# Optimization experiments

Hardware: AMD Instinct MI355X
Metric: run time of the kernel (lower is better)

## Reference

```python
import jax, jax.numpy as jnp
import numpy as np
from jax.ops import segment_sum, segment_max

NEG_SLOPE = 0.2  # PyG GATv2Conv default

def _gatv2(x, ei, ea, Wl, bl, Wr, br, We, att, b, n):
    # PyG GATv2Conv, heads=1, concat=True, add_self_loops=True, fill_value='mean'
    src, dst = ei[0], ei[1]
    ones = jnp.ones((src.shape[0],), x.dtype)
    deg = segment_sum(ones, dst, num_segments=n)
    ea_mean = segment_sum(ea, dst, num_segments=n) / jnp.maximum(deg, 1.0)[:, None]
    loop = jnp.arange(n, dtype=src.dtype)
    src = jnp.concatenate([src, loop]); dst = jnp.concatenate([dst, loop])
    ea = jnp.concatenate([ea, ea_mean], axis=0)
    xl = x @ Wl.T + bl          # lin_l, used for both message and source term
    xr = x @ Wr.T + br          # lin_r, target term
    h = jax.nn.leaky_relu(xl[src] + xr[dst] + ea @ We.T, NEG_SLOPE)  # [E+N, F]
    logits = h @ att            # [E+N]
    m = segment_max(logits, dst, num_segments=n)   # every node has a self-loop -> finite
    p = jnp.exp(logits - m[dst])
    denom = segment_sum(p, dst, num_segments=n)
    alpha = p / denom[dst]
    return segment_sum(alpha[:, None] * xl[src], dst, num_segments=n) + b

def _mean_pool(h, seg, num):
    s = segment_sum(h, seg, num_segments=num)
    c = segment_sum(jnp.ones(h.shape[:1], h.dtype), seg, num_segments=num)
    return s / jnp.maximum(c, 1.0)[:, None]

def setup_inputs() -> dict:
    key = jax.random.key(0)
    ks = iter(jax.random.split(key, 64))
    def nrm(shape, scale=None):
        s = scale if scale is not None else 1.0 / np.sqrt(shape[-1])
        return jax.random.normal(next(ks), shape, jnp.float32) * s
    N, E = 80000, 1280000
    NR, ER, R = 20480, 40960, 512
    inp = {
        'x': nrm((N, 16), 1.0),
        'edge_attr': nrm((E, 18), 1.0),
        'rule_x': nrm((NR, 16), 1.0),
        'rule_edge_attr': nrm((ER, 18), 1.0),
    }
    def gat(fi, fo):
        return (nrm((fo, fi)), jnp.zeros(fo), nrm((fo, fi)), jnp.zeros(fo),
                nrm((fo, 18)), nrm((fo,), 1.0 / np.sqrt(fo)), jnp.zeros(fo))
    for name, (fi, fo) in [('gat0', (16, 100)), ('gat1', (16, 100)), ('gat2', (100, 200))]:
        for suf, v in zip(['Wl', 'bl', 'Wr', 'br', 'We', 'att', 'b'], gat(fi, fo)):
            inp[name + '_' + suf] = v
    inp['lin_W'] = nrm((400, 200)); inp['lin_b'] = jnp.zeros(400)
    inp['f1_W'] = nrm((200, 400)); inp['f1_b'] = jnp.zeros(200)
    inp['f2_W'] = nrm((100, 200)); inp['f2_b'] = jnp.zeros(100)
    inp['f3_W'] = nrm((100, 100)); inp['f3_b'] = jnp.zeros(100)
    inp['bil_W'] = nrm((1, 100, 100)); inp['bil_b'] = jnp.zeros(1)
    inp['edge_index'] = jax.random.randint(next(ks), (2, E), 0, N, dtype=jnp.int32)
    inp['batch'] = jnp.zeros((N,), jnp.int32)
    inp['rule_edge_index'] = jax.random.randint(next(ks), (2, ER), 0, NR, dtype=jnp.int32)
    inp['rule_batch'] = jnp.sort(jax.random.randint(next(ks), (NR,), 0, R, dtype=jnp.int32))
    inp['n_rules'] = R
    return inp

def reference(x, edge_attr, rule_x, rule_edge_attr,
              gat0_Wl, gat0_bl, gat0_Wr, gat0_br, gat0_We, gat0_att, gat0_b,
              gat1_Wl, gat1_bl, gat1_Wr, gat1_br, gat1_We, gat1_att, gat1_b,
              gat2_Wl, gat2_bl, gat2_Wr, gat2_br, gat2_We, gat2_att, gat2_b,
              lin_W, lin_b, f1_W, f1_b, f2_W, f2_b, f3_W, f3_b, bil_W, bil_b,
              edge_index, batch, rule_edge_index, rule_batch, n_rules):
    N = x.shape[0]; NR = rule_x.shape[0]
    # --- RuleParse path ---
    h = jax.nn.relu(_gatv2(rule_x, rule_edge_index, rule_edge_attr,
                           gat1_Wl, gat1_bl, gat1_Wr, gat1_br, gat1_We, gat1_att, gat1_b, NR))
    h = jax.nn.relu(_gatv2(h, rule_edge_index, rule_edge_attr,
                           gat2_Wl, gat2_bl, gat2_Wr, gat2_br, gat2_We, gat2_att, gat2_b, NR))
    h = h @ lin_W.T + lin_b                          # [NR, 400]
    y = _mean_pool(h, rule_batch, n_rules)           # [R, 400]
    y = jax.nn.relu(y @ f1_W.T + f1_b)
    y = jax.nn.relu(y @ f2_W.T + f2_b)
    y = y @ f3_W.T + f3_b                            # [R, 100]
    # --- data path ---
    g = _gatv2(x, edge_index, edge_attr,
               gat0_Wl, gat0_bl, gat0_Wr, gat0_br, gat0_We, gat0_att, gat0_b, N)
    xp = _mean_pool(g, batch, 1)                     # single graph -> [1, 100]
    xr = jnp.tile(xp, (n_rules, 1))                  # x.repeat(len(rules), 1)
    out = jnp.einsum('nd,ode,ne->no', xr, bil_W, y) + bil_b  # Bilinear(100,100,1) -> [R,1]
    return out.T.squeeze()                           # [R]
```

## Files before the change

### kernel.cpp

```cpp
#include <hip/hip_runtime.h>

#define NS 0.2f

__global__ void k_deg(const int* __restrict__ dst, int* degi, int E){
  int stride = gridDim.x * blockDim.x;
  for(int e = blockIdx.x * blockDim.x + threadIdx.x; e < E; e += stride)
    atomicAdd(&degi[dst[e]], 1);
}

__device__ __forceinline__ int wave_iscan(int v, int lane){
  #pragma unroll
  for(int o = 1; o < 64; o <<= 1){
    int t = __shfl_up(v, o);
    if(lane >= o) v += t;
  }
  return v;
}

__global__ __launch_bounds__(1024) void k_scan_sum(
    const int* __restrict__ deg, int* __restrict__ bsum, int n)
{
  __shared__ int wsum[16];
  const int lane = threadIdx.x & 63;
  const int w = threadIdx.x >> 6;
  int idx = blockIdx.x * 1024 + threadIdx.x;
  int v = (idx < n) ? deg[idx] : 0;
  #pragma unroll
  for(int o = 32; o; o >>= 1) v += __shfl_xor(v, o);
  if(lane == 0) wsum[w] = v;
  __syncthreads();
  if(w == 0){
    int s = (lane < 16) ? wsum[lane] : 0;
    #pragma unroll
    for(int o = 8; o; o >>= 1) s += __shfl_xor(s, o);
    if(lane == 0) bsum[blockIdx.x] = s;
  }
}

__global__ __launch_bounds__(128) void k_scan_bsum(
    int* __restrict__ bsum, int* __restrict__ rowoff, int B, int n)
{
  __shared__ int wtot[2];
  const int lane = threadIdx.x & 63;
  const int w = threadIdx.x >> 6;
  int t = threadIdx.x;
  int v = (t < B) ? bsum[t] : 0;
  int inc = wave_iscan(v, lane);
  if(lane == 63) wtot[w] = inc;
  __syncthreads();
  int off = (w > 0) ? wtot[0] : 0;
  if(t < B) bsum[t] = off + inc - v;
  if(t == 0) rowoff[n] = wtot[0] + wtot[1];
}

__global__ __launch_bounds__(1024) void k_scan_apply(
    const int* __restrict__ deg, const int* __restrict__ bsum,
    int* __restrict__ rowoff, int* __restrict__ pos, int n)
{
  __shared__ int wsum[16];
  const int lane = threadIdx.x & 63;
  const int w = threadIdx.x >> 6;
  int idx = blockIdx.x * 1024 + threadIdx.x;
  int v = (idx < n) ? deg[idx] : 0;
  int inc = wave_iscan(v, lane);
  if(lane == 63) wsum[w] = inc;
  __syncthreads();
  if(w == 0){
    int s = (lane < 16) ? wsum[lane] : 0;
    s = wave_iscan(s, lane);
    if(lane < 16) wsum[lane] = s;
  }
  __syncthreads();
  int woff = (w > 0) ? wsum[w - 1] : 0;
  if(idx < n){
    int ex = bsum[blockIdx.x] + woff + inc - v;
    rowoff[idx] = ex;
    pos[idx] = ex;
  }
}

__global__ void k_fill(const int* __restrict__ dst, int* pos, int* eidx, int E){
  int stride = gridDim.x * blockDim.x;
  for(int e = blockIdx.x * blockDim.x + threadIdx.x; e < E; e += stride){
    int slot = atomicAdd(&pos[dst[e]], 1);
    eidx[slot] = e;
  }
}

__global__ __launch_bounds__(256) void k_easum(
    const float* __restrict__ ea, const int* __restrict__ rowoff,
    const int* __restrict__ eidx, float* __restrict__ eam, int n)
{
  const int lane = threadIdx.x & 63;
  const int wid  = threadIdx.x >> 6;
  const int i = blockIdx.x * 4 + wid;
  if(i >= n) return;
  const int r0 = rowoff[i], r1 = rowoff[i + 1];
  const int deg = r1 - r0;
  const int pg = lane / 18;
  const int k  = lane - pg * 18;
  float s = 0.0f;
  if(pg < 3){
    for(int p = r0 + pg; p < r1; p += 3)
      s += ea[(long)eidx[p] * 18 + k];
  }
  float b = __shfl(s, lane + 18);
  float c = __shfl(s, lane + 36);
  if(lane < 18) eam[(long)i * 18 + lane] = (s + b + c) / fmaxf((float)deg, 1.0f);
}

#define BM 64
#define BN 64
#define BK 16
__global__ __launch_bounds__(256) void k_gemm(
    const float* __restrict__ A, const float* __restrict__ W,
    const float* __restrict__ b, float* __restrict__ C,
    int n, int K, int M, int dorelu)
{
  __shared__ float As[BK][BM + 4];
  __shared__ float Bs[BK][BN + 4];
  const int bi = blockIdx.x * BM;
  const int bj = blockIdx.y * BN;
  const int tid = threadIdx.x;
  const int tr = tid / 16, tc = tid % 16;
  float acc[4][4] = {};
  for(int k0 = 0; k0 < K; k0 += BK){
    for(int l = tid; l < BM * BK; l += 256){
      int c = l % BK, r = l / BK;
      int gr = bi + r, gc = k0 + c;
      As[c][r] = (gr < n && gc < K) ? A[(long)gr * K + gc] : 0.0f;
    }
    for(int l = tid; l < BN * BK; l += 256){
      int c = l % BK, r = l / BK;
      int gr = bj + r, gc = k0 + c;
      Bs[c][r] = (gr < M && gc < K) ? W[(long)gr * K + gc] : 0.0f;
    }
    __syncthreads();
    #pragma unroll
    for(int kk = 0; kk < BK; ++kk){
      float4 av = *(const float4*)&As[kk][tr * 4];
      float4 bv = *(const float4*)&Bs[kk][tc * 4];
      acc[0][0] = fmaf(av.x, bv.x, acc[0][0]); acc[0][1] = fmaf(av.x, bv.y, acc[0][1]);
      acc[0][2] = fmaf(av.x, bv.z, acc[0][2]); acc[0][3] = fmaf(av.x, bv.w, acc[0][3]);
      acc[1][0] = fmaf(av.y, bv.x, acc[1][0]); acc[1][1] = fmaf(av.y, bv.y, acc[1][1]);
      acc[1][2] = fmaf(av.y, bv.z, acc[1][2]); acc[1][3] = fmaf(av.y, bv.w, acc[1][3]);
      acc[2][0] = fmaf(av.z, bv.x, acc[2][0]); acc[2][1] = fmaf(av.z, bv.y, acc[2][1]);
      acc[2][2] = fmaf(av.z, bv.z, acc[2][2]); acc[2][3] = fmaf(av.z, bv.w, acc[2][3]);
      acc[3][0] = fmaf(av.w, bv.x, acc[3][0]); acc[3][1] = fmaf(av.w, bv.y, acc[3][1]);
      acc[3][2] = fmaf(av.w, bv.z, acc[3][2]); acc[3][3] = fmaf(av.w, bv.w, acc[3][3]);
    }
    __syncthreads();
  }
  for(int r = 0; r < 4; r++){
    int gr = bi + tr * 4 + r;
    if(gr >= n) continue;
    for(int c = 0; c < 4; c++){
      int gc = bj + tc * 4 + c;
      if(gc >= M) continue;
      float val = acc[r][c] + b[gc];
      C[(long)gr * M + gc] = dorelu ? fmaxf(val, 0.0f) : val;
    }
  }
}

static void gemm_launch(const float* A, const float* W, const float* b, float* C,
                        int n, int K, int M, int relu, hipStream_t s){
  dim3 grid((n + BM - 1) / BM, (M + BN - 1) / BN);
  k_gemm<<<grid, 256, 0, s>>>(A, W, b, C, n, K, M, relu);
}

__device__ __forceinline__ float lkrelu(float t){ return (t > 0.0f) ? t : NS * t; }

template<int G, int F>
__global__ __launch_bounds__(256) void k_edge_logits(
    const float* __restrict__ xl, const float* __restrict__ xr,
    const float* __restrict__ ea,
    const int* __restrict__ src, const int* __restrict__ dst,
    const int* __restrict__ eidx,
    const float* __restrict__ We, const float* __restrict__ att,
    float2* __restrict__ lw, int E)
{
  constexpr int NG = 256 / G;
  constexpr int NE = 4;
  constexpr int FQ = F / 4;
  __shared__ float4 sWeT[18 * FQ];
  __shared__ float4 sAtt[FQ];
  __shared__ float4 sEa[NG][18];
  __shared__ int    sIdx[NG][3][NE];

  const int tid = threadIdx.x;
  for(int idx = tid; idx < F * 18; idx += 256){
    int f = idx / 18, k = idx % 18;
    ((float*)sWeT)[k * F + f] = We[idx];
  }
  for(int f = tid; f < F; f += 256) ((float*)sAtt)[f] = att[f];
  __syncthreads();

  const int g  = tid / G;
  const int gl = tid % G;
  const bool act = (gl * 4 < F);
  const int glc = act ? gl : 0;
  const long step = (long)gridDim.x * (NG * NE);

  for(long base = (long)blockIdx.x * (NG * NE); base < (long)E; base += step){
    const long pb = base + (long)g * NE;
    if(gl < NE){
      long p = pb + gl;
      int e = -1, s = 0, d = 0;
      if(p < (long)E){ e = eidx[p]; s = src[e]; d = dst[e]; }
      sIdx[g][0][gl] = e; sIdx[g][1][gl] = s; sIdx[g][2][gl] = d;
    }
    #pragma unroll
    for(int t = 0; t < (9 * NE + G - 1) / G; ++t){
      int u = t * G + gl;
      if(u < 9 * NE){
        int ne = u & 3, k2 = u >> 2;
        int e = sIdx[g][0][ne];
        float2 v = (e >= 0) ? *(const float2*)(ea + (long)e * 18 + k2 * 2)
                            : make_float2(0.0f, 0.0f);
        ((float*)&sEa[g][k2 * 2 + 0])[ne] = v.x;
        ((float*)&sEa[g][k2 * 2 + 1])[ne] = v.y;
      }
    }
    int4 sv = *(const int4*)&sIdx[g][1][0];
    int4 dv = *(const int4*)&sIdx[g][2][0];
    float4 a0 = *(const float4*)(xl + (long)sv.x * F + glc * 4);
    float4 b0 = *(const float4*)(xr + (long)dv.x * F + glc * 4);
    float4 a1 = *(const float4*)(xl + (long)sv.y * F + glc * 4);
    float4 b1 = *(const float4*)(xr + (long)dv.y * F + glc * 4);
    float4 a2 = *(const float4*)(xl + (long)sv.z * F + glc * 4);
    float4 b2 = *(const float4*)(xr + (long)dv.z * F + glc * 4);
    float4 a3 = *(const float4*)(xl + (long)sv.w * F + glc * 4);
    float4 b3 = *(const float4*)(xr + (long)dv.w * F + glc * 4);
    float4 t0 = make_float4(a0.x + b0.x, a0.y + b0.y, a0.z + b0.z, a0.w + b0.w);
    float4 t1 = make_float4(a1.x + b1.x, a1.y + b1.y, a1.z + b1.z, a1.w + b1.w);
    float4 t2 = make_float4(a2.x + b2.x, a2.y + b2.y, a2.z + b2.z, a2.w + b2.w);
    float4 t3 = make_float4(a3.x + b3.x, a3.y + b3.y, a3.z + b3.z, a3.w + b3.w);
    #pragma unroll
    for(int k = 0; k < 18; ++k){
      float4 w  = sWeT[k * FQ + glc];
      float4 eq = sEa[g][k];
      t0.x = fmaf(w.x, eq.x, t0.x); t0.y = fmaf(w.y, eq.x, t0.y);
      t0.z = fmaf(w.z, eq.x, t0.z); t0.w = fmaf(w.w, eq.x, t0.w);
      t1.x = fmaf(w.x, eq.y, t1.x); t1.y = fmaf(w.y, eq.y, t1.y);
      t1.z = fmaf(w.z, eq.y, t1.z); t1.w = fmaf(w.w, eq.y, t1.w);
      t2.x = fmaf(w.x, eq.z, t2.x); t2.y = fmaf(w.y, eq.z, t2.y);
      t2.z = fmaf(w.z, eq.z, t2.z); t2.w = fmaf(w.w, eq.z, t2.w);
      t3.x = fmaf(w.x, eq.w, t3.x); t3.y = fmaf(w.y, eq.w, t3.y);
      t3.z = fmaf(w.z, eq.w, t3.z); t3.w = fmaf(w.w, eq.w, t3.w);
    }
    float4 av = sAtt[glc];
    float r0 = 0, r1 = 0, r2 = 0, r3 = 0;
    if(act){
      r0 = av.x * lkrelu(t0.x) + av.y * lkrelu(t0.y) + av.z * lkrelu(t0.z) + av.w * lkrelu(t0.w);
      r1 = av.x * lkrelu(t1.x) + av.y * lkrelu(t1.y) + av.z * lkrelu(t1.z) + av.w * lkrelu(t1.w);
      r2 = av.x * lkrelu(t2.x) + av.y * lkrelu(t2.y) + av.z * lkrelu(t2.z) + av.w * lkrelu(t2.w);
      r3 = av.x * lkrelu(t3.x) + av.y * lkrelu(t3.y) + av.z * lkrelu(t3.z) + av.w * lkrelu(t3.w);
    }
    #pragma unroll
    for(int o = G / 2; o; o >>= 1){
      r0 += __shfl_xor(r0, o);
      r1 += __shfl_xor(r1, o);
      r2 += __shfl_xor(r2, o);
      r3 += __shfl_xor(r3, o);
    }
    if(gl == 0 && pb + 0 < (long)E) lw[pb + 0] = make_float2(r0, __int_as_float(sv.x));
    if(gl == 1 && pb + 1 < (long)E) lw[pb + 1] = make_float2(r1, __int_as_float(sv.y));
    if(gl == 2 && pb + 2 < (long)E) lw[pb + 2] = make_float2(r2, __int_as_float(sv.z));
    if(gl == 3 && pb + 3 < (long)E) lw[pb + 3] = make_float2(r3, __int_as_float(sv.w));
  }
}

#define CH 128
template<int JMAX>
__global__ __launch_bounds__(256) void k_gat_agg(
    const float* __restrict__ xl, const float* __restrict__ xr,
    const float* __restrict__ eam,
    const float* __restrict__ We, const float* __restrict__ att,
    const int* __restrict__ rowoff, const float2* __restrict__ lw,
    const float* __restrict__ bias, float* __restrict__ out,
    int n, int F, int dorelu)
{
  const int lane = threadIdx.x & 63;
  const int wid  = threadIdx.x >> 6;
  __shared__ float2 s_ws[4][CH];
  const int i = blockIdx.x * 4 + wid;
  if(i >= n) return;
  const int r0 = rowoff[i], r1 = rowoff[i + 1];
  const int deg = r1 - r0;

  float eamv[18];
  #pragma unroll
  for(int k = 0; k < 18; ++k) eamv[k] = eam[(long)i * 18 + k];

  float selfl = 0.0f;
  float acc[JMAX];
  #pragma unroll
  for(int j = 0; j < JMAX; ++j){
    int f = lane + j * 64;
    float xv = (f < F) ? xl[(long)i * F + f] : 0.0f;
    acc[j] = xv;
    if(f < F){
      float t = xv + xr[(long)i * F + f];
      const float* w = We + f * 18;
      #pragma unroll
      for(int k = 0; k < 18; ++k) t = fmaf(w[k], eamv[k], t);
      t = lkrelu(t);
      selfl = fmaf(att[f], t, selfl);
    }
  }
  #pragma unroll
  for(int o = 32; o; o >>= 1) selfl += __shfl_xor(selfl, o);

  float m = selfl, denom = 1.0f;

  for(int c0 = 0; c0 < deg; c0 += CH){
    int cn = min(CH, deg - c0);
    float lmax = -3.4e38f;
    for(int q = lane; q < cn; q += 64){
      float2 ws = lw[r0 + c0 + q];
      s_ws[wid][q] = ws;
      lmax = fmaxf(lmax, ws.x);
    }
    #pragma unroll
    for(int o = 32; o; o >>= 1) lmax = fmaxf(lmax, __shfl_xor(lmax, o));
    float newm = fmaxf(m, lmax);
    float scale = __expf(m - newm);
    denom *= scale;
    #pragma unroll
    for(int j = 0; j < JMAX; ++j) acc[j] *= scale;
    m = newm;
    float psum = 0.0f;
    for(int q = lane; q < cn; q += 64){
      float2 ws = s_ws[wid][q];
      float w = __expf(ws.x - m);
      s_ws[wid][q].x = w;
      psum += w;
    }
    #pragma unroll
    for(int o = 32; o; o >>= 1) psum += __shfl_xor(psum, o);
    denom += psum;
    int p = 0;
    for(; p + 8 <= cn; p += 8){
      float2 wv[8];
      const float* xs[8];
      #pragma unroll
      for(int u = 0; u < 8; ++u){
        wv[u] = s_ws[wid][p + u];
        xs[u] = xl + (long)__float_as_int(wv[u].y) * F;
      }
      float vv[8][JMAX];
      #pragma unroll
      for(int u = 0; u < 8; ++u)
        #pragma unroll
        for(int j = 0; j < JMAX; ++j){
          int f = lane + j * 64;
          vv[u][j] = (f < F) ? xs[u][f] : 0.0f;
        }
      #pragma unroll
      for(int u = 0; u < 8; ++u)
        #pragma unroll
        for(int j = 0; j < JMAX; ++j)
          acc[j] = fmaf(wv[u].x, vv[u][j], acc[j]);
    }
    for(; p < cn; ++p){
      float2 ws = s_ws[wid][p];
      const float* xs = xl + (long)__float_as_int(ws.y) * F;
      #pragma unroll
      for(int j = 0; j < JMAX; ++j){
        int f = lane + j * 64;
        if(f < F) acc[j] = fmaf(ws.x, xs[f], acc[j]);
      }
    }
  }

  float inv = 1.0f / denom;
  #pragma unroll
  for(int j = 0; j < JMAX; ++j){
    int f = lane + j * 64;
    if(f < F){
      float o = acc[j] * inv + bias[f];
      out[(long)i * F + f] = dorelu ? fmaxf(o, 0.0f) : o;
    }
  }
}

__global__ void k_rule_starts(const int* __restrict__ rb, int* starts, int NR, int R){
  int r = blockIdx.x * blockDim.x + threadIdx.x;
  if(r > R) return;
  if(r == R){ starts[R] = NR; return; }
  int lo = 0, hi = NR;
  while(lo < hi){ int mid = (lo + hi) >> 1; if(rb[mid] < r) lo = mid + 1; else hi = mid; }
  starts[r] = lo;
}

__global__ void k_pool_rules(const float* __restrict__ h, const int* __restrict__ starts,
                             float* __restrict__ y, int R, int F){
  long idx = (long)blockIdx.x * blockDim.x + threadIdx.x;
  long total = (long)R * F;
  if(idx >= total) return;
  int r = (int)(idx / F);
  int f = (int)(idx % F);
  int s0 = starts[r], s1 = starts[r + 1];
  float a = 0.0f;
  for(int i = s0; i < s1; i++) a += h[(long)i * F + f];
  y[idx] = a / fmaxf((float)(s1 - s0), 1.0f);
}

__global__ __launch_bounds__(256) void k_pool_all(
    const float* __restrict__ g, float* xp, int n, int F)
{
  const int lane = threadIdx.x & 63;
  const int wid  = threadIdx.x >> 6;
  const int nw   = 4;
  float a0 = 0.0f, a1 = 0.0f;
  const bool ok0 = lane < F, ok1 = lane + 64 < F;
  for(int r = blockIdx.x * nw + wid; r < n; r += gridDim.x * nw){
    const float* row = g + (long)r * F;
    if(ok0) a0 += row[lane];
    if(ok1) a1 += row[lane + 64];
  }
  __shared__ float s[4][128];
  s[wid][lane] = a0;
  s[wid][lane + 64] = a1;
  __syncthreads();
  if(wid == 0){
    float t0 = s[0][lane] + s[1][lane] + s[2][lane] + s[3][lane];
    float t1 = s[0][lane + 64] + s[1][lane + 64] + s[2][lane + 64] + s[3][lane + 64];
    if(ok0 && t0 != 0.0f) atomicAdd(&xp[lane], t0);
    if(ok1 && t1 != 0.0f) atomicAdd(&xp[lane + 64], t1);
  }
}

__global__ __launch_bounds__(512) void k_bil(
    const float* __restrict__ xp, const float* __restrict__ Wb,
    const float* __restrict__ y, const float* __restrict__ bilb,
    float* __restrict__ out, float inv_n, int R)
{
  __shared__ float v[100];
  int t = threadIdx.x;
  if(t < 100){
    float a = 0.0f;
    for(int d = 0; d < 100; d++) a += xp[d] * Wb[d * 100 + t];
    v[t] = a * inv_n;
  }
  __syncthreads();
  for(int r = t; r < R; r += 512){
    float a = 0.0f;
    const float* yr = y + (long)r * 100;
    for(int e = 0; e < 100; e++) a += v[e] * yr[e];
    out[r] = a + bilb[0];
  }
}

static inline int nblk(long n){
  long b = (n + 255) / 256;
  if(b > 20480) b = 20480;
  if(b < 1) b = 1;
  return (int)b;
}

struct GatParams { const float *Wl,*bl,*Wr,*br,*We,*att,*b; };

template<int G, int F>
static void logits_launch(const float* xl, const float* xr, const float* ea,
                          const int* src, const int* dst, const int* eidx,
                          const float* We, const float* att, float2* lw,
                          int E, hipStream_t stream){
  const int epb = (256 / G) * 4;
  long nb = ((long)E + epb - 1) / epb;
  int grid = (int)(nb < 2048 ? nb : 2048);
  k_edge_logits<G, F><<<grid, 256, 0, stream>>>(xl, xr, ea, src, dst, eidx, We, att, lw, E);
}

static void scan_launch(const int* degi, int* bsum, int* rowoff, int* pos,
                        int n, hipStream_t stream){
  int B = (n + 1023) / 1024;
  k_scan_sum  <<<B, 1024, 0, stream>>>(degi, bsum, n);
  k_scan_bsum <<<1, 128,  0, stream>>>(bsum, rowoff, B, n);
  k_scan_apply<<<B, 1024, 0, stream>>>(degi, bsum, rowoff, pos, n);
}

static void run_gatv2(const float* x, int fin, int fout, int n,
                      const int* src, const int* dst, const float* ea, int E,
                      GatParams P, float* out, int dorelu,
                      float* xl, float* xr, float2* lw,
                      const float* eam, const int* rowoff, const int* eidx,
                      hipStream_t stream){
  gemm_launch(x, P.Wl, P.bl, xl, n, fin, fout, 0, stream);
  gemm_launch(x, P.Wr, P.br, xr, n, fin, fout, 0, stream);
  if(fout == 100){
    logits_launch<32, 100>(xl, xr, ea, src, dst, eidx, P.We, P.att, lw, E, stream);
    k_gat_agg<2><<<(n + 3) / 4, 256, 0, stream>>>(xl, xr, eam, P.We, P.att,
                                                  rowoff, lw, P.b, out, n, fout, dorelu);
  } else {
    logits_launch<64, 200>(xl, xr, ea, src, dst, eidx, P.We, P.att, lw, E, stream);
    k_gat_agg<4><<<(n + 3) / 4, 256, 0, stream>>>(xl, xr, eam, P.We, P.att,
                                                  rowoff, lw, P.b, out, n, fout, dorelu);
  }
}

extern "C" void kernel_launch(void* const* d_in, const int* in_sizes, int n_in,
                              void* d_out, int out_size, void* d_ws, size_t ws_size,
                              hipStream_t stream){
  const float* x   = (const float*)d_in[0];
  const float* ea  = (const float*)d_in[1];
  const float* rx  = (const float*)d_in[2];
  const float* rea = (const float*)d_in[3];
  GatParams g0{ (const float*)d_in[4],  (const float*)d_in[5],  (const float*)d_in[6],
                (const float*)d_in[7],  (const float*)d_in[8],  (const float*)d_in[9],
                (const float*)d_in[10] };
  GatParams g1{ (const float*)d_in[11], (const float*)d_in[12], (const float*)d_in[13],
                (const float*)d_in[14], (const float*)d_in[15], (const float*)d_in[16],
                (const float*)d_in[17] };
  GatParams g2{ (const float*)d_in[18], (const float*)d_in[19], (const float*)d_in[20],
                (const float*)d_in[21], (const float*)d_in[22], (const float*)d_in[23],
                (const float*)d_in[24] };
  const float* lin_W = (const float*)d_in[25]; const float* lin_b = (const float*)d_in[26];
  const float* f1_W  = (const float*)d_in[27]; const float* f1_b  = (const float*)d_in[28];
  const float* f2_W  = (const float*)d_in[29]; const float* f2_b  = (const float*)d_in[30];
  const float* f3_W  = (const float*)d_in[31]; const float* f3_b  = (const float*)d_in[32];
  const float* bilW  = (const float*)d_in[33]; const float* bilb  = (const float*)d_in[34];
  const int* ei  = (const int*)d_in[35];
  const int* rei = (const int*)d_in[37];
  const int* rb  = (const int*)d_in[38];

  const int N  = in_sizes[0] / 16;
  const int E  = in_sizes[1] / 18;
  const int NR = in_sizes[2] / 16;
  const int ER = in_sizes[3] / 18;
  const int R  = out_size;

  float* Wf = (float*)d_ws;
  size_t off = 0;
  auto alloc  = [&](size_t nf){ nf = (nf + 1) & ~(size_t)1; float* p = Wf + off; off += nf; return p; };
  auto alloci = [&](size_t ni){ ni = (ni + 1) & ~(size_t)1; int* p = (int*)(Wf + off); off += ni; return p; };

  float* y0 = alloc((size_t)R * 400);
  float* y1 = alloc((size_t)R * 200);
  float* y2 = alloc((size_t)R * 100);
  float* y3 = alloc((size_t)R * 100);
  float* xp = alloc(128);
  int* starts = alloci(R + 1);
  const size_t arena = off;

  {
    off = arena;
    float* h1 = alloc((size_t)NR * 100);
    float* h2 = alloc((size_t)NR * 200);
    float* xl = alloc((size_t)NR * 200);
    float* xr = alloc((size_t)NR * 200);
    float2* lw = (float2*)alloc((size_t)ER * 2);
    float* eam   = alloc((size_t)NR * 18);
    int* rowoff = alloci(NR + 1);
    int* degi   = alloci(NR);
    int* pos    = alloci(NR);
    int* bsum   = alloci(128);
    int* eidx   = alloci(ER);
    const int* rsrc = rei; const int* rdst = rei + ER;

    hipMemsetAsync(degi, 0, (size_t)NR * 4, stream);
    k_deg<<<nblk(ER), 256, 0, stream>>>(rdst, degi, ER);
    scan_launch(degi, bsum, rowoff, pos, NR, stream);
    k_fill<<<nblk(ER), 256, 0, stream>>>(rdst, pos, eidx, ER);
    k_easum<<<(NR + 3) / 4, 256, 0, stream>>>(rea, rowoff, eidx, eam, NR);

    run_gatv2(rx, 16, 100, NR, rsrc, rdst, rea, ER, g1, h1, 1,
              xl, xr, lw, eam, rowoff, eidx, stream);
    run_gatv2(h1, 100, 200, NR, rsrc, rdst, rea, ER, g2, h2, 1,
              xl, xr, lw, eam, rowoff, eidx, stream);

    float* hlin = xl;
    gemm_launch(h2, lin_W, lin_b, hlin, NR, 200, 400, 0, stream);

    k_rule_starts<<<(R + 256) / 256, 256, 0, stream>>>(rb, starts, NR, R);
    k_pool_rules<<<nblk((long)R * 400), 256, 0, stream>>>(hlin, starts, y0, R, 400);

    gemm_launch(y0, f1_W, f1_b, y1, R, 400, 200, 1, stream);
    gemm_launch(y1, f2_W, f2_b, y2, R, 200, 100, 1, stream);
    gemm_launch(y2, f3_W, f3_b, y3, R, 100, 100, 0, stream);
  }

  {
    off = arena;
    float* g  = alloc((size_t)N * 100);
    float* xl = alloc((size_t)N * 100);
    float* xr = alloc((size_t)N * 100);
    float2* lw = (float2*)alloc((size_t)E * 2);
    float* eam   = alloc((size_t)N * 18);
    int* rowoff = alloci((size_t)N + 1);
    int* degi   = alloci(N);
    int* pos    = alloci(N);
    int* bsum   = alloci(128);
    int* eidx   = alloci(E);
    const int* srcp = ei; const int* dstp = ei + E;

    hipMemsetAsync(degi, 0, (size_t)N * 4, stream);
    k_deg<<<nblk(E), 256, 0, stream>>>(dstp, degi, E);
    scan_launch(degi, bsum, rowoff, pos, N, stream);
    k_fill<<<nblk(E), 256, 0, stream>>>(dstp, pos, eidx, E);
    k_easum<<<(N + 3) / 4, 256, 0, stream>>>(ea, rowoff, eidx, eam, N);

    run_gatv2(x, 16, 100, N, srcp, dstp, ea, E, g0, g, 0,
              xl, xr, lw, eam, rowoff, eidx, stream);

    hipMemsetAsync(xp, 0, 128 * 4, stream);
    k_pool_all<<<1024, 256, 0, stream>>>(g, xp, N, 100);
    k_bil<<<1, 512, 0, stream>>>(xp, bilW, y3, bilb, (float*)d_out, 1.0f / (float)N, R);
  }
}
```

Measured before the change: 1.032 ms.

## Store data-path GAT node projections in fp16 and add half-precision edge/aggregation kernels

For the large data graph, the xl/xr node projections are now written as fp16 by a new GEMM variant. New edge-logit and aggregation kernels gather these half-precision rows, which halves the bytes moved by the random per-edge gathers that dominate this layer. The edge-logit kernel also keeps We in registers instead of shared memory and fixes the group size to 32 for F=100. The cost is lower precision in the projected features, which could shift logits and outputs slightly.

```diff
diff --git a/kernel.cpp b/kernel.cpp
--- a/kernel.cpp
+++ b/kernel.cpp
@@ -1,4 +1,5 @@
 #include <hip/hip_runtime.h>
+#include <hip/hip_fp16.h>
 
 #define NS 0.2f
 
@@ -163,10 +164,78 @@
   }
 }
 
+__global__ __launch_bounds__(256) void k_gemm_h(
+    const float* __restrict__ A, const float* __restrict__ W,
+    const float* __restrict__ b, __half* __restrict__ C,
+    int n, int K, int M)
+{
+  __shared__ float As[BK][BM + 4];
+  __shared__ float Bs[BK][BN + 4];
+  const int bi = blockIdx.x * BM;
+  const int bj = blockIdx.y * BN;
+  const int tid = threadIdx.x;
+  const int tr = tid / 16, tc = tid % 16;
+  float acc[4][4] = {};
+  for(int k0 = 0; k0 < K; k0 += BK){
+    for(int l = tid; l < BM * BK; l += 256){
+      int c = l % BK, r = l / BK;
+      int gr = bi + r, gc = k0 + c;
+      As[c][r] = (gr < n && gc < K) ? A[(long)gr * K + gc] : 0.0f;
+    }
+    for(int l = tid; l < BN * BK; l += 256){
+      int c = l % BK, r = l / BK;
+      int gr = bj + r, gc = k0 + c;
+      Bs[c][r] = (gr < M && gc < K) ? W[(long)gr * K + gc] : 0.0f;
+    }
+    __syncthreads();
+    #pragma unroll
+    for(int kk = 0; kk < BK; ++kk){
+      float4 av = *(const float4*)&As[kk][tr * 4];
+      float4 bv = *(const float4*)&Bs[kk][tc * 4];
+      acc[0][0] = fmaf(av.x, bv.x, acc[0][0]); acc[0][1] = fmaf(av.x, bv.y, acc[0][1]);
+      acc[0][2] = fmaf(av.x, bv.z, acc[0][2]); acc[0][3] = fmaf(av.x, bv.w, acc[0][3]);
+      acc[1][0] = fmaf(av.y, bv.x, acc[1][0]); acc[1][1] = fmaf(av.y, bv.y, acc[1][1]);
+      acc[1][2] = fmaf(av.y, bv.z, acc[1][2]); acc[1][3] = fmaf(av.y, bv.w, acc[1][3]);
+      acc[2][0] = fmaf(av.z, bv.x, acc[2][0]); acc[2][1] = fmaf(av.z, bv.y, acc[2][1]);
+      acc[2][2] = fmaf(av.z, bv.z, acc[2][2]); acc[2][3] = fmaf(av.z, bv.w, acc[2][3]);
+      acc[3][0] = fmaf(av.w, bv.x, acc[3][0]); acc[3][1] = fmaf(av.w, bv.y, acc[3][1]);
+      acc[3][2] = fmaf(av.w, bv.z, acc[3][2]); acc[3][3] = fmaf(av.w, bv.w, acc[3][3]);
+    }
+    __syncthreads();
+  }
+  for(int r = 0; r < 4; r++){
+    int gr = bi + tr * 4 + r;
+    if(gr >= n) continue;
+    int gc0 = bj + tc * 4;
+    float v[4];
+    #pragma unroll
+    for(int c = 0; c < 4; c++){
+      int gc = gc0 + c;
+      v[c] = (gc < M) ? acc[r][c] + b[gc] : 0.0f;
+    }
+    __half* Crow = C + (long)gr * M;
+    if(gc0 + 3 < M){
+      *(__half2*)(Crow + gc0)     = __halves2half2(__float2half(v[0]), __float2half(v[1]));
+      *(__half2*)(Crow + gc0 + 2) = __halves2half2(__float2half(v[2]), __float2half(v[3]));
+    } else {
+      for(int c = 0; c < 4; c++){
+        int gc = gc0 + c;
+        if(gc < M) Crow[gc] = __float2half(v[c]);
+      }
+    }
+  }
+}
+
 static void gemm_launch(const float* A, const float* W, const float* b, float* C,
                         int n, int K, int M, int relu, hipStream_t s){
   dim3 grid((n + BM - 1) / BM, (M + BN - 1) / BN);
   k_gemm<<<grid, 256, 0, s>>>(A, W, b, C, n, K, M, relu);
+}
+
+static void gemm_h_launch(const float* A, const float* W, const float* b, __half* C,
+                          int n, int K, int M, hipStream_t s){
+  dim3 grid((n + BM - 1) / BM, (M + BN - 1) / BN);
+  k_gemm_h<<<grid, 256, 0, s>>>(A, W, b, C, n, K, M);
 }
 
 __device__ __forceinline__ float lkrelu(float t){ return (t > 0.0f) ? t : NS * t; }
@@ -250,6 +319,106 @@
       t3.z = fmaf(w.z, eq.w, t3.z); t3.w = fmaf(w.w, eq.w, t3.w);
     }
     float4 av = sAtt[glc];
+    float r0 = 0, r1 = 0, r2 = 0, r3 = 0;
+    if(act){
+      r0 = av.x * lkrelu(t0.x) + av.y * lkrelu(t0.y) + av.z * lkrelu(t0.z) + av.w * lkrelu(t0.w);
+      r1 = av.x * lkrelu(t1.x) + av.y * lkrelu(t1.y) + av.z * lkrelu(t1.z) + av.w * lkrelu(t1.w);
+      r2 = av.x * lkrelu(t2.x) + av.y * lkrelu(t2.y) + av.z * lkrelu(t2.z) + av.w * lkrelu(t2.w);
+      r3 = av.x * lkrelu(t3.x) + av.y * lkrelu(t3.y) + av.z * lkrelu(t3.z) + av.w * lkrelu(t3.w);
+    }
+    #pragma unroll
+    for(int o = G / 2; o; o >>= 1){
+      r0 += __shfl_xor(r0, o);
+      r1 += __shfl_xor(r1, o);
+      r2 += __shfl_xor(r2, o);
+      r3 += __shfl_xor(r3, o);
+    }
+    if(gl == 0 && pb + 0 < (long)E) lw[pb + 0] = make_float2(r0, __int_as_float(sv.x));
+    if(gl == 1 && pb + 1 < (long)E) lw[pb + 1] = make_float2(r1, __int_as_float(sv.y));
+    if(gl == 2 && pb + 2 < (long)E) lw[pb + 2] = make_float2(r2, __int_as_float(sv.z));
+    if(gl == 3 && pb + 3 < (long)E) lw[pb + 3] = make_float2(r3, __int_as_float(sv.w));
+  }
+}
+
+__global__ __launch_bounds__(256) void k_edge_logits_h(
+    const __half* __restrict__ xl, const __half* __restrict__ xr,
+    const float* __restrict__ ea,
+    const int* __restrict__ src, const int* __restrict__ dst,
+    const int* __restrict__ eidx,
+    const float* __restrict__ We, const float* __restrict__ att,
+    float2* __restrict__ lw, int E)
+{
+  constexpr int G = 32, NG = 8, NE = 4, F = 100;
+  __shared__ float4 sEa[NG][18];
+  __shared__ int    sIdx[NG][3][NE];
+
+  const int tid = threadIdx.x;
+  const int g  = tid / G;
+  const int gl = tid % G;
+  const bool act = (gl * 4 < F);
+  const int glc = act ? gl : 0;
+
+  float4 wreg[18];
+  #pragma unroll
+  for(int k = 0; k < 18; ++k){
+    wreg[k].x = We[(glc * 4 + 0) * 18 + k];
+    wreg[k].y = We[(glc * 4 + 1) * 18 + k];
+    wreg[k].z = We[(glc * 4 + 2) * 18 + k];
+    wreg[k].w = We[(glc * 4 + 3) * 18 + k];
+  }
+  const float4 av = make_float4(att[glc * 4 + 0], att[glc * 4 + 1],
+                                att[glc * 4 + 2], att[glc * 4 + 3]);
+
+  const long step = (long)gridDim.x * (NG * NE);
+  for(long base = (long)blockIdx.x * (NG * NE); base < (long)E; base += step){
+    const long pb = base + (long)g * NE;
+    if(gl < NE){
+      long p = pb + gl;
+      int e = -1, s = 0, d = 0;
+      if(p < (long)E){ e = eidx[p]; s = src[e]; d = dst[e]; }
+      sIdx[g][0][gl] = e; sIdx[g][1][gl] = s; sIdx[g][2][gl] = d;
+    }
+    #pragma unroll
+    for(int t = 0; t < 2; ++t){
+      int u = t * G + gl;
+      if(u < 9 * NE){
+        int ne = u & 3, k2 = u >> 2;
+        int e = sIdx[g][0][ne];
+        float2 v = (e >= 0) ? *(const float2*)(ea + (long)e * 18 + k2 * 2)
+                            : make_float2(0.0f, 0.0f);
+        ((float*)&sEa[g][k2 * 2 + 0])[ne] = v.x;
+        ((float*)&sEa[g][k2 * 2 + 1])[ne] = v.y;
+      }
+    }
+    int4 sv = *(const int4*)&sIdx[g][1][0];
+    int4 dv = *(const int4*)&sIdx[g][2][0];
+    auto ld4h = [&](const __half* base_p, int row) -> float4 {
+      const __half2* p = (const __half2*)(base_p + (long)row * F + glc * 4);
+      float2 lo = __half22float2(p[0]);
+      float2 hi = __half22float2(p[1]);
+      return make_float4(lo.x, lo.y, hi.x, hi.y);
+    };
+    float4 a0 = ld4h(xl, sv.x), b0 = ld4h(xr, dv.x);
+    float4 a1 = ld4h(xl, sv.y), b1 = ld4h(xr, dv.y);
+    float4 a2 = ld4h(xl, sv.z), b2 = ld4h(xr, dv.z);
+    float4 a3 = ld4h(xl, sv.w), b3 = ld4h(xr, dv.w);
+    float4 t0 = make_float4(a0.x + b0.x, a0.y + b0.y, a0.z + b0.z, a0.w + b0.w);
+    float4 t1 = make_float4(a1.x + b1.x, a1.y + b1.y, a1.z + b1.z, a1.w + b1.w);
+    float4 t2 = make_float4(a2.x + b2.x, a2.y + b2.y, a2.z + b2.z, a2.w + b2.w);
+    float4 t3 = make_float4(a3.x + b3.x, a3.y + b3.y, a3.z + b3.z, a3.w + b3.w);
+    #pragma unroll
+    for(int k = 0; k < 18; ++k){
+      float4 w  = wreg[k];
+      float4 eq = sEa[g][k];
+      t0.x = fmaf(w.x, eq.x, t0.x); t0.y = fmaf(w.y, eq.x, t0.y);
+      t0.z = fmaf(w.z, eq.x, t0.z); t0.w = fmaf(w.w, eq.x, t0.w);
+      t1.x = fmaf(w.x, eq.y, t1.x); t1.y = fmaf(w.y, eq.y, t1.y);
+      t1.z = fmaf(w.z, eq.y, t1.z); t1.w = fmaf(w.w, eq.y, t1.w);
+      t2.x = fmaf(w.x, eq.z, t2.x); t2.y = fmaf(w.y, eq.z, t2.y);
+      t2.z = fmaf(w.z, eq.z, t2.z); t2.w = fmaf(w.w, eq.z, t2.w);
+      t3.x = fmaf(w.x, eq.w, t3.x); t3.y = fmaf(w.y, eq.w, t3.y);
+      t3.z = fmaf(w.z, eq.w, t3.z); t3.w = fmaf(w.w, eq.w, t3.w);
+    }
     float r0 = 0, r1 = 0, r2 = 0, r3 = 0;
     if(act){
       r0 = av.x * lkrelu(t0.x) + av.y * lkrelu(t0.y) + av.z * lkrelu(t0.z) + av.w * lkrelu(t0.w);
@@ -385,6 +554,111 @@
   }
 }
 
+__global__ __launch_bounds__(256) void k_gat_agg_h(
+    const __half* __restrict__ xl, const __half* __restrict__ xr,
+    const float* __restrict__ eam,
+    const float* __restrict__ We, const float* __restrict__ att,
+    const int* __restrict__ rowoff, const float2* __restrict__ lw,
+    const float* __restrict__ bias, float* __restrict__ out, int n)
+{
+  constexpr int F = 100;
+  const int lane = threadIdx.x & 63;
+  const int wid  = threadIdx.x >> 6;
+  __shared__ float2 s_ws[4][CH];
+  const int i = blockIdx.x * 4 + wid;
+  if(i >= n) return;
+  const int r0 = rowoff[i], r1 = rowoff[i + 1];
+  const int deg = r1 - r0;
+  const bool okq = lane < 50;
+  const int q = okq ? lane : 0;
+
+  float eamv[18];
+  #pragma unroll
+  for(int k = 0; k < 18; ++k) eamv[k] = eam[(long)i * 18 + k];
+
+  float2 xo = make_float2(0.0f, 0.0f);
+  float selfl = 0.0f;
+  if(okq){
+    xo = __half22float2(((const __half2*)(xl + (long)i * F))[q]);
+    float2 xro = __half22float2(((const __half2*)(xr + (long)i * F))[q]);
+    int f0 = 2 * q, f1 = 2 * q + 1;
+    float t0 = xo.x + xro.x, t1 = xo.y + xro.y;
+    const float* w0 = We + f0 * 18;
+    const float* w1 = We + f1 * 18;
+    #pragma unroll
+    for(int k = 0; k < 18; ++k){
+      t0 = fmaf(w0[k], eamv[k], t0);
+      t1 = fmaf(w1[k], eamv[k], t1);
+    }
+    t0 = lkrelu(t0); t1 = lkrelu(t1);
+    selfl = att[f0] * t0 + att[f1] * t1;
+  }
+  #pragma unroll
+  for(int o = 32; o; o >>= 1) selfl += __shfl_xor(selfl, o);
+
+  float m = selfl, denom = 1.0f;
+  float acc0 = xo.x, acc1 = xo.y;
+
+  for(int c0 = 0; c0 < deg; c0 += CH){
+    int cn = min(CH, deg - c0);
+    float lmax = -3.4e38f;
+    for(int p = lane; p < cn; p += 64){
+      float2 ws = lw[r0 + c0 + p];
+      s_ws[wid][p] = ws;
+      lmax = fmaxf(lmax, ws.x);
+    }
+    #pragma unroll
+    for(int o = 32; o; o >>= 1) lmax = fmaxf(lmax, __shfl_xor(lmax, o));
+    float newm = fmaxf(m, lmax);
+    float scale = __expf(m - newm);
+    denom *= scale; acc0 *= scale; acc1 *= scale;
+    m = newm;
+    float psum = 0.0f;
+    for(int p = lane; p < cn; p += 64){
+      float2 ws = s_ws[wid][p];
+      float w = __expf(ws.x - m);
+      s_ws[wid][p].x = w;
+      psum += w;
+    }
+    #pragma unroll
+    for(int o = 32; o; o >>= 1) psum += __shfl_xor(psum, o);
+    denom += psum;
+    int p = 0;
+    for(; p + 8 <= cn; p += 8){
+      float2 wv[8];
+      const __half2* xs[8];
+      #pragma unroll
+      for(int u = 0; u < 8; ++u){
+        wv[u] = s_ws[wid][p + u];
+        xs[u] = (const __half2*)(xl + (long)__float_as_int(wv[u].y) * F);
+      }
+      float2 vv[8];
+      #pragma unroll
+      for(int u = 0; u < 8; ++u)
+        vv[u] = okq ? __half22float2(xs[u][q]) : make_float2(0.0f, 0.0f);
+      #pragma unroll
+      for(int u = 0; u < 8; ++u){
+        acc0 = fmaf(wv[u].x, vv[u].x, acc0);
+        acc1 = fmaf(wv[u].x, vv[u].y, acc1);
+      }
+    }
+    for(; p < cn; ++p){
+      float2 ws = s_ws[wid][p];
+      const __half2* xs = (const __half2*)(xl + (long)__float_as_int(ws.y) * F);
+      float2 v = okq ? __half22float2(xs[q]) : make_float2(0.0f, 0.0f);
+      acc0 = fmaf(ws.x, v.x, acc0);
+      acc1 = fmaf(ws.x, v.y, acc1);
+    }
+  }
+
+  if(okq){
+    float inv = 1.0f / denom;
+    float2 bv = *(const float2*)(bias + 2 * q);
+    float2 ov = make_float2(acc0 * inv + bv.x, acc1 * inv + bv.y);
+    *(float2*)(out + (long)i * F + 2 * q) = ov;
+  }
+}
+
 __global__ void k_rule_starts(const int* __restrict__ rb, int* starts, int NR, int R){
   int r = blockIdx.x * blockDim.x + threadIdx.x;
   if(r > R) return;
@@ -584,8 +858,8 @@
   {
     off = arena;
     float* g  = alloc((size_t)N * 100);
-    float* xl = alloc((size_t)N * 100);
-    float* xr = alloc((size_t)N * 100);
+    __half* xlh = (__half*)alloc((size_t)N * 50);
+    __half* xrh = (__half*)alloc((size_t)N * 50);
     float2* lw = (float2*)alloc((size_t)E * 2);
     float* eam   = alloc((size_t)N * 18);
     int* rowoff = alloci((size_t)N + 1);
@@ -601,8 +875,16 @@
     k_fill<<<nblk(E), 256, 0, stream>>>(dstp, pos, eidx, E);
     k_easum<<<(N + 3) / 4, 256, 0, stream>>>(ea, rowoff, eidx, eam, N);
 
-    run_gatv2(x, 16, 100, N, srcp, dstp, ea, E, g0, g, 0,
-              xl, xr, lw, eam, rowoff, eidx, stream);
+    gemm_h_launch(x, g0.Wl, g0.bl, xlh, N, 16, 100, stream);
+    gemm_h_launch(x, g0.Wr, g0.br, xrh, N, 16, 100, stream);
+    {
+      long nb = ((long)E + 31) / 32;
+      int grid = (int)(nb < 2048 ? nb : 2048);
+      k_edge_logits_h<<<grid, 256, 0, stream>>>(xlh, xrh, ea, srcp, dstp, eidx,
+                                                g0.We, g0.att, lw, E);
+    }
+    k_gat_agg_h<<<(N + 3) / 4, 256, 0, stream>>>(xlh, xrh, eam, g0.We, g0.att,
+                                                 rowoff, lw, g0.b, g, N);
 
     hipMemsetAsync(xp, 0, 128 * 4, stream);
     k_pool_all<<<1024, 256, 0, stream>>>(g, xp, N, 100);
```

New measurement: 1.315 ms. 1.27x slower.
